# Optimization experiments

Measured on AMD Instinct MI355X. Metric: run time of the kernel, lower is better.

Reference implementation:

```python
import jax, jax.numpy as jnp
import numpy as np

N = 50000      # nodes per graph
E = 800000     # directed edges per graph
D_IN, C1, C2, C3, K = 96, 64, 32, 16, 16  # K = tensor_neurons (Linear(16,16) forces 16)


def setup_inputs() -> dict:
    key = jax.random.key(0)
    ks = jax.random.split(key, 18)
    def w(k, shape, scale=0.1):
        return (jax.random.normal(k, shape, jnp.float32) * scale)
    return {
        "features_1": jax.random.normal(ks[0], (N, D_IN), jnp.float32),
        "features_2": jax.random.normal(ks[1], (N, D_IN), jnp.float32),
        "edges_1": jax.random.randint(ks[2], (2, E), 0, N),
        "edges_2": jax.random.randint(ks[3], (2, E), 0, N),
        # GCN layer params (PyG GCNConv: X @ W then normalized aggregation, then + b)
        "W1": w(ks[4], (D_IN, C1)), "b1": jnp.zeros((C1,), jnp.float32),
        "W2": w(ks[5], (C1, C2)),  "b2": jnp.zeros((C2,), jnp.float32),
        "W3": w(ks[6], (C2, C3)),  "b3": jnp.zeros((C3,), jnp.float32),
        # Attention pooling weight matrix [C3, C3]
        "Wa": w(ks[7], (C3, C3)),
        # Tensor network: bilinear tensor [C3, C3, K], block [K, 2*C3], bias [K]
        "Wt": w(ks[8], (C3, C3, K)),
        "Wb": w(ks[9], (K, 2 * C3)),
        "bt": w(ks[10], (K,)),
        # fully_connected_first Linear(16,16) and scoring Linear(16,1)
        "Wfc": w(ks[11], (K, 16)), "bfc": jnp.zeros((16,), jnp.float32),
        "Wsc": w(ks[12], (16, 1)), "bsc": jnp.zeros((1,), jnp.float32),
    }


def gcn_conv(x, src, dst, W, b):
    # PyG GCNConv with self-loops: D^-1/2 (A+I) D^-1/2 (X W) + b
    h = x @ W                                   # [N, C]
    ones = jnp.ones(src.shape[0], h.dtype)
    deg = jax.ops.segment_sum(ones, dst, num_segments=N) + 1.0   # in-degree + self loop
    dinv = jax.lax.rsqrt(deg)                   # [N]
    coef = dinv[src] * dinv[dst]                # [E]
    agg = jax.ops.segment_sum(h[src] * coef[:, None], dst, num_segments=N)
    return agg + h * (dinv * dinv)[:, None] + b  # self-loop term has norm dinv_i^2


def encode(x, edges, W1, b1, W2, b2, W3, b3):
    src, dst = edges[0], edges[1]
    x = jax.nn.relu(gcn_conv(x, src, dst, W1, b1))  # dropout is a no-op in eval mode
    x = jax.nn.relu(gcn_conv(x, src, dst, W2, b2))
    return gcn_conv(x, src, dst, W3, b3)


def attention_pool(x, Wa):
    # SimGNN AttentionModule: c = tanh(mean(x Wa)); s = sigmoid(x c); rep = x^T s
    c = jnp.tanh(jnp.mean(x @ Wa, axis=0))      # [C3]
    s = jax.nn.sigmoid(x @ c)                   # [N]
    return x.T @ s                              # [C3]


def reference(features_1, features_2, edges_1, edges_2,
              W1, b1, W2, b2, W3, b3, Wa, Wt, Wb, bt, Wfc, bfc, Wsc, bsc):
    h1 = encode(features_1, edges_1, W1, b1, W2, b2, W3, b3)
    h2 = encode(features_2, edges_2, W1, b1, W2, b2, W3, b3)
    e1 = attention_pool(h1, Wa)                 # [C3]
    e2 = attention_pool(h2, Wa)                 # [C3]
    # Tensor network scoring
    bilinear = jnp.einsum('i,ijk,j->k', e1, Wt, e2)        # [K]
    block = Wb @ jnp.concatenate([e1, e2])                 # [K]
    scores = jax.nn.relu(bilinear + block + bt)            # [K]
    scores = jnp.tanh(scores @ Wfc + bfc)                  # [16]
    score = jax.nn.sigmoid(scores @ Wsc + bsc)             # [1]
    return score
```

## Files before the change

### kernel.cpp

```cpp
#include <hip/hip_runtime.h>
#include <hip/hip_bf16.h>

#define TPB 256
#define SH 6
#define BW 64

typedef unsigned short u16;
typedef __attribute__((ext_vector_type(8))) __bf16 bf16x8;
typedef __attribute__((ext_vector_type(4))) float f32x4;

__device__ __forceinline__ u16 f_to_bf(float f) {
    unsigned u = __float_as_uint(f);
    return (u16)((u + 0x7fff + ((u >> 16) & 1)) >> 16);
}
__device__ __forceinline__ float4 bf4_to_f4(ushort4 v) {
    float4 r;
    r.x = __uint_as_float((unsigned)v.x << 16);
    r.y = __uint_as_float((unsigned)v.y << 16);
    r.z = __uint_as_float((unsigned)v.z << 16);
    r.w = __uint_as_float((unsigned)v.w << 16);
    return r;
}
__device__ __forceinline__ void facc(float4& a, float4 v) {
    a.x += v.x; a.y += v.y; a.z += v.z; a.w += v.w;
}
__device__ __forceinline__ float4 shfl_xor4(float4 v, int mask, int width) {
    v.x = __shfl_xor(v.x, mask, width);
    v.y = __shfl_xor(v.y, mask, width);
    v.z = __shfl_xor(v.z, mask, width);
    v.w = __shfl_xor(v.w, mask, width);
    return v;
}

__device__ __forceinline__ bool swz_block(int nblk, int& g, int& bx) {
    int blk = blockIdx.x;
    int j = blk & 7;
    g = j >> 2;
    bx = (blk >> 3) * 4 + (j & 3);
    return bx < nblk;
}

template <int C>
__device__ __forceinline__ float4 gather_sum(const u16* __restrict__ HW,
                                             const int* __restrict__ col,
                                             int c0, int ps, int pe) {
    float4 a0 = make_float4(0.f, 0.f, 0.f, 0.f);
    float4 a1 = a0, a2 = a0, a3 = a0;
    int p = ps;
    for (; p + 8 <= pe; p += 8) {
        int j[8];
        ushort4 d[8];
#pragma unroll
        for (int k = 0; k < 8; k++) j[k] = col[p + k];
#pragma unroll
        for (int k = 0; k < 8; k++) d[k] = *(const ushort4*)&HW[(size_t)j[k] * C + c0];
        facc(a0, bf4_to_f4(d[0])); facc(a1, bf4_to_f4(d[1]));
        facc(a2, bf4_to_f4(d[2])); facc(a3, bf4_to_f4(d[3]));
        facc(a0, bf4_to_f4(d[4])); facc(a1, bf4_to_f4(d[5]));
        facc(a2, bf4_to_f4(d[6])); facc(a3, bf4_to_f4(d[7]));
    }
    if (p + 4 <= pe) {
        int j[4];
        ushort4 d[4];
#pragma unroll
        for (int k = 0; k < 4; k++) j[k] = col[p + k];
#pragma unroll
        for (int k = 0; k < 4; k++) d[k] = *(const ushort4*)&HW[(size_t)j[k] * C + c0];
        facc(a0, bf4_to_f4(d[0])); facc(a1, bf4_to_f4(d[1]));
        facc(a2, bf4_to_f4(d[2])); facc(a3, bf4_to_f4(d[3]));
        p += 4;
    }
    for (; p < pe; p++) {
        int j = col[p];
        facc(a0, bf4_to_f4(*(const ushort4*)&HW[(size_t)j * C + c0]));
    }
    facc(a0, a1); facc(a2, a3); facc(a0, a2);
    return a0;
}


__global__ void bucket_scatter_kernel(const int* __restrict__ e0, const int* __restrict__ e1,
                                      int E, int* __restrict__ bcur,
                                      int* __restrict__ ebuf0, int* __restrict__ ebuf1,
                                      int nbuk, int cap) {
    int g = blockIdx.y;
    const int* src = g ? e1 : e0;
    const int* dst = src + E;
    int* ebuf = g ? ebuf1 : ebuf0;
    int* bu = bcur + g * 1024;
    __shared__ int hist[1024];
    for (int t = threadIdx.x; t < 1024; t += TPB) hist[t] = 0;
    __syncthreads();
    int base = blockIdx.x * 4096;
    int pk[16], bk[16], rk[16];
#pragma unroll
    for (int k = 0; k < 16; k++) {
        int e = base + k * TPB + (int)threadIdx.x;
        bk[k] = -1;
        if (e < E) {
            int s = src[e], d = dst[e];
            int b = d >> SH;
            bk[k] = b;
            pk[k] = (s << SH) | (d & (BW - 1));
            rk[k] = atomicAdd(&hist[b], 1);
        }
    }
    __syncthreads();
    for (int t = threadIdx.x; t < nbuk; t += TPB) {
        int h = hist[t];
        hist[t] = h ? atomicAdd(&bu[t], h) : 0;
    }
    __syncthreads();
#pragma unroll
    for (int k = 0; k < 16; k++)
        if (bk[k] >= 0) {
            int pos = hist[bk[k]] + rk[k];
            if (pos < cap) ebuf[(size_t)bk[k] * cap + pos] = pk[k];
        }
}

__global__ void bucket_csr_kernel(const int* __restrict__ ebuf0, const int* __restrict__ ebuf1,
                                  const int* __restrict__ bcur, int n, int cap,
                                  int* __restrict__ soff0, int* __restrict__ soff1,
                                  int* __restrict__ eoff0, int* __restrict__ eoff1,
                                  float* __restrict__ dinv0, float* __restrict__ dinv1,
                                  int* __restrict__ col0, int* __restrict__ col1) {
    int g = blockIdx.y;
    int b = blockIdx.x;
    const int* ebuf = g ? ebuf1 : ebuf0;
    int* soff = g ? soff1 : soff0;
    int* eoff = g ? eoff1 : eoff0;
    float* dinv = g ? dinv1 : dinv0;
    int* col = g ? col1 : col0;
    __shared__ int h[BW], nb[BW], nrank[BW];
    int tid = threadIdx.x;
    if (tid < BW) h[tid] = 0;
    __syncthreads();
    int s = b * cap;
    int cnt = min(bcur[g * 1024 + b], cap);
    int e = s + cnt;
    for (int i = s + tid; i < e; i += TPB)
        atomicAdd(&h[ebuf[i] & (BW - 1)], 1);
    __syncthreads();
    if (tid < BW) {
        int v = h[tid];
        int x = v;
        for (int d = 1; d < BW; d <<= 1) {
            int u = __shfl_up(x, d, 64);
            if (tid >= d) x += u;
        }
        int base = s + x - v;
        nb[tid] = base;
        nrank[tid] = 0;
        int node = b * BW + tid;
        if (node < n) {
            soff[node] = base;
            eoff[node] = base + v;
            dinv[node] = rsqrtf((float)v + 1.0f);
        }
    }
    __syncthreads();
    for (int i = s + tid; i < e; i += TPB) {
        int p = ebuf[i];
        int lo = p & (BW - 1);
        int r = atomicAdd(&nrank[lo], 1);
        col[nb[lo] + r] = p >> SH;
    }
}


template <int CIN, int COUT>
__global__ void matmul_kernel(const float* __restrict__ X0, const float* __restrict__ X1,
                              const float* __restrict__ W,
                              const float* __restrict__ dinv0, const float* __restrict__ dinv1,
                              u16* __restrict__ Y0, u16* __restrict__ Y1, int n) {
    constexpr int CINP = CIN + 8;
    constexpr int NT = COUT / 16;
    constexpr int KT = CIN / 32;
    __shared__ u16 Xs[64 * CINP];
    __shared__ u16 Wt[COUT * CINP];

    int g = blockIdx.y;
    const float* X = g ? X1 : X0;
    const float* dinv = g ? dinv1 : dinv0;
    u16* Y = g ? Y1 : Y0;
    int nb0 = blockIdx.x * 64;

    for (int i = threadIdx.x; i < 64 * (CIN / 4); i += TPB) {
        int nn = i / (CIN / 4), kc = i % (CIN / 4);
        float4 v = make_float4(0.f, 0.f, 0.f, 0.f);
        if (nb0 + nn < n) v = *(const float4*)&X[(size_t)(nb0 + nn) * CIN + 4 * kc];
        ushort4 b;
        b.x = f_to_bf(v.x); b.y = f_to_bf(v.y); b.z = f_to_bf(v.z); b.w = f_to_bf(v.w);
        *(ushort4*)&Xs[nn * CINP + 4 * kc] = b;
    }
    for (int i = threadIdx.x; i < CIN * (COUT / 4); i += TPB) {
        int k = i / (COUT / 4), nc4 = i % (COUT / 4);
        float4 v = *(const float4*)&W[(size_t)k * COUT + 4 * nc4];
        Wt[(4 * nc4 + 0) * CINP + k] = f_to_bf(v.x);
        Wt[(4 * nc4 + 1) * CINP + k] = f_to_bf(v.y);
        Wt[(4 * nc4 + 2) * CINP + k] = f_to_bf(v.z);
        Wt[(4 * nc4 + 3) * CINP + k] = f_to_bf(v.w);
    }
    __syncthreads();

    int lane = threadIdx.x & 63;
    int w = threadIdx.x >> 6;
    int m = lane & 15;
    int quad = lane >> 4;

    f32x4 acc[NT];
#pragma unroll
    for (int t = 0; t < NT; t++) acc[t] = (f32x4){0.f, 0.f, 0.f, 0.f};
#pragma unroll
    for (int kt = 0; kt < KT; kt++) {
        int k0 = kt * 32 + quad * 8;
        bf16x8 a = *(const bf16x8*)&Xs[(w * 16 + m) * CINP + k0];
#pragma unroll
        for (int t = 0; t < NT; t++) {
            bf16x8 b = *(const bf16x8*)&Wt[(t * 16 + m) * CINP + k0];
            acc[t] = __builtin_amdgcn_mfma_f32_16x16x32_bf16(a, b, acc[t], 0, 0, 0);
        }
    }
#pragma unroll
    for (int r = 0; r < 4; r++) {
        int node = nb0 + w * 16 + quad * 4 + r;
        if (node < n) {
            float d = dinv[node];
#pragma unroll
            for (int t = 0; t < NT; t++)
                Y[(size_t)node * COUT + t * 16 + m] = f_to_bf(acc[t][r] * d);
        }
    }
}


template <int C, int SPLIT, int COUT2>
__global__ __launch_bounds__(TPB, 2)
void agg_mm_kernel(const u16* __restrict__ HW0, const u16* __restrict__ HW1,
                   const int* __restrict__ soff0, const int* __restrict__ soff1,
                   const int* __restrict__ eoff0, const int* __restrict__ eoff1,
                   const int* __restrict__ col0, const int* __restrict__ col1,
                   const float* __restrict__ dinv0, const float* __restrict__ dinv1,
                   const float* __restrict__ bias, const float* __restrict__ W2,
                   u16* __restrict__ Y0, u16* __restrict__ Y1, int n, int nblk) {
    constexpr int CH = C / 4;
    constexpr int TPN = CH * SPLIT;
    constexpr int CP = C + 8;
    constexpr int NT2 = COUT2 / 16;
    constexpr int KT2 = C / 32;
    __shared__ __align__(16) u16 HsB[16 * CP];
    __shared__ __align__(16) u16 WtB[COUT2 * CP];

    int g, bx;
    if (!swz_block(nblk, g, bx)) return;
    const u16* HW = g ? HW1 : HW0;
    const int* soff = g ? soff1 : soff0;
    const int* eoff = g ? eoff1 : eoff0;
    const int* col = g ? col1 : col0;
    const float* dinv = g ? dinv1 : dinv0;
    u16* Y = g ? Y1 : Y0;

    for (int idx = threadIdx.x; idx < C * COUT2; idx += TPB) {
        int k = idx / COUT2, nc = idx % COUT2;
        WtB[nc * CP + k] = f_to_bf(W2[idx]);
    }

    int tid = bx * TPB + (int)threadIdx.x;
    int node = tid / TPN;
    int nl = threadIdx.x / TPN;
    int part = threadIdx.x % TPN;
    int sp = part / CH;
    int c0 = (part % CH) * 4;
    float4 o = make_float4(0.f, 0.f, 0.f, 0.f);
    if (node < n) {
        int s = soff[node], e = eoff[node];
        int len = e - s;
        int chunk = (len + SPLIT - 1) / SPLIT;
        int ps = s + sp * chunk;
        int pe = min(ps + chunk, e);
        float4 r = gather_sum<C>(HW, col, c0, ps, pe);
#pragma unroll
        for (int m = CH; m < TPN; m <<= 1) facc(r, shfl_xor4(r, m, TPN));
        if (sp == 0) {
            float di = dinv[node];
            float4 self = bf4_to_f4(*(const ushort4*)&HW[(size_t)node * C + c0]);
            float4 b4 = *(const float4*)&bias[c0];
            o.x = fmaxf(di * (r.x + self.x) + b4.x, 0.f);
            o.y = fmaxf(di * (r.y + self.y) + b4.y, 0.f);
            o.z = fmaxf(di * (r.z + self.z) + b4.z, 0.f);
            o.w = fmaxf(di * (r.w + self.w) + b4.w, 0.f);
        }
    }
    if (sp == 0) {
        ushort4 hb;
        hb.x = f_to_bf(o.x); hb.y = f_to_bf(o.y); hb.z = f_to_bf(o.z); hb.w = f_to_bf(o.w);
        *(ushort4*)&HsB[nl * CP + c0] = hb;
    }
    __syncthreads();

    int lane = threadIdx.x & 63;
    int w = threadIdx.x >> 6;
    if (w < NT2) {
        int m = lane & 15;
        int quad = lane >> 4;
        f32x4 acc = (f32x4){0.f, 0.f, 0.f, 0.f};
#pragma unroll
        for (int kt = 0; kt < KT2; kt++) {
            int k0 = kt * 32 + quad * 8;
            bf16x8 a = *(const bf16x8*)&HsB[m * CP + k0];
            bf16x8 b = *(const bf16x8*)&WtB[(w * 16 + m) * CP + k0];
            acc = __builtin_amdgcn_mfma_f32_16x16x32_bf16(a, b, acc, 0, 0, 0);
        }
        int base16 = bx * 16;
#pragma unroll
        for (int r = 0; r < 4; r++) {
            int onode = base16 + quad * 4 + r;
            if (onode < n)
                Y[(size_t)onode * COUT2 + w * 16 + m] = f_to_bf(acc[r] * dinv[onode]);
        }
    }
}

__global__ __launch_bounds__(TPB, 2)
void agg16_kernel(const u16* __restrict__ HW0, const u16* __restrict__ HW1,
                  const int* __restrict__ soff0, const int* __restrict__ soff1,
                  const int* __restrict__ eoff0, const int* __restrict__ eoff1,
                  const int* __restrict__ col0, const int* __restrict__ col1,
                  const float* __restrict__ dinv0, const float* __restrict__ dinv1,
                  const float* __restrict__ bias,
                  float* __restrict__ out0, float* __restrict__ out1,
                  float* __restrict__ pcol, int n, int nblk) {
    int g, bx;
    if (!swz_block(nblk, g, bx)) return;
    const u16* HW = g ? HW1 : HW0;
    const int* soff = g ? soff1 : soff0;
    const int* eoff = g ? eoff1 : eoff0;
    const int* col = g ? col1 : col0;
    const float* dinv = g ? dinv1 : dinv0;
    float* outp = g ? out1 : out0;
    int tid = bx * TPB + (int)threadIdx.x;
    int node = tid / 16;
    int part = tid % 16;
    int sp = part / 4;
    int c0 = (part % 4) * 4;
    float4 o = make_float4(0.f, 0.f, 0.f, 0.f);
    if (node < n) {
        int s = soff[node], e = eoff[node];
        int len = e - s;
        int chunk = (len + 3) / 4;
        int ps = s + sp * chunk;
        int pe = min(ps + chunk, e);
        float4 r = gather_sum<16>(HW, col, c0, ps, pe);
        facc(r, shfl_xor4(r, 4, 16));
        facc(r, shfl_xor4(r, 8, 16));
        if (sp == 0) {
            float di = dinv[node];
            float4 self = bf4_to_f4(*(const ushort4*)&HW[(size_t)node * 16 + c0]);
            float4 b4 = *(const float4*)&bias[c0];
            o.x = di * (r.x + self.x) + b4.x;
            o.y = di * (r.y + self.y) + b4.y;
            o.z = di * (r.z + self.z) + b4.z;
            o.w = di * (r.w + self.w) + b4.w;
            *(float4*)&outp[(size_t)node * 16 + c0] = o;
        }
    }
    __shared__ float4 sd[TPB];
    sd[threadIdx.x] = (node < n && sp == 0) ? o : make_float4(0.f, 0.f, 0.f, 0.f);
    __syncthreads();
    if (threadIdx.x < 64) {
        float4 a = sd[threadIdx.x];
        facc(a, sd[threadIdx.x + 64]);
        facc(a, sd[threadIdx.x + 128]);
        facc(a, sd[threadIdx.x + 192]);
        sd[threadIdx.x] = a;
    }
    __syncthreads();
    if (threadIdx.x < 16) {
        float4 a = sd[threadIdx.x];
        facc(a, sd[threadIdx.x + 16]);
        facc(a, sd[threadIdx.x + 32]);
        facc(a, sd[threadIdx.x + 48]);
        sd[threadIdx.x] = a;
    }
    __syncthreads();
    if (threadIdx.x < 4)
        *(float4*)&pcol[((size_t)g * nblk + bx) * 16 + threadIdx.x * 4] = sd[threadIdx.x];
}


__global__ void cvec_kernel(const float* __restrict__ pcol, int nb16, float n_inv,
                            const float* __restrict__ Wa, float* __restrict__ cvec) {
    int g = blockIdx.x;
    const float4* p4 = (const float4*)(pcol + (size_t)g * nb16 * 16);
    __shared__ float4 sd[TPB];
    __shared__ float cs[16];
    int c4 = threadIdx.x & 3;
    int row = threadIdx.x >> 2;
    float4 acc = make_float4(0.f, 0.f, 0.f, 0.f);
    for (int r = row; r < nb16; r += 64) facc(acc, p4[(size_t)r * 4 + c4]);
    sd[threadIdx.x] = acc;
    __syncthreads();
    if (threadIdx.x < 64) {
        float4 a = sd[threadIdx.x];
        facc(a, sd[threadIdx.x + 64]);
        facc(a, sd[threadIdx.x + 128]);
        facc(a, sd[threadIdx.x + 192]);
        sd[threadIdx.x] = a;
    }
    __syncthreads();
    if (threadIdx.x < 16) {
        float4 a = sd[threadIdx.x];
        facc(a, sd[threadIdx.x + 16]);
        facc(a, sd[threadIdx.x + 32]);
        facc(a, sd[threadIdx.x + 48]);
        sd[threadIdx.x] = a;
    }
    __syncthreads();
    if (threadIdx.x < 4) {
        float4 a = sd[threadIdx.x];
        facc(a, sd[threadIdx.x + 4]);
        facc(a, sd[threadIdx.x + 8]);
        facc(a, sd[threadIdx.x + 12]);
        cs[threadIdx.x * 4 + 0] = a.x * n_inv;
        cs[threadIdx.x * 4 + 1] = a.y * n_inv;
        cs[threadIdx.x * 4 + 2] = a.z * n_inv;
        cs[threadIdx.x * 4 + 3] = a.w * n_inv;
    }
    __syncthreads();
    if (threadIdx.x < 16) {
        float acc2 = 0.f;
#pragma unroll
        for (int i = 0; i < 16; i++) acc2 += cs[i] * Wa[i * 16 + threadIdx.x];
        cvec[g * 16 + threadIdx.x] = tanhf(acc2);
    }
}


__global__ void pool_kernel(const float* __restrict__ H0, const float* __restrict__ H1, int n,
                            const float* __restrict__ cvec, float* __restrict__ ppool) {
    int g = blockIdx.y;
    const float* H = g ? H1 : H0;
    int c = threadIdx.x & 15;
    float cv = cvec[g * 16 + c];
    int w = (blockIdx.x * blockDim.x + threadIdx.x) / 16;
    int stride = (gridDim.x * blockDim.x) / 16;
    float acc = 0.f;
    for (int node = w; node < n; node += stride) {
        float x = H[(size_t)node * 16 + c];
        float p = x * cv;
        p += __shfl_xor(p, 1, 16);
        p += __shfl_xor(p, 2, 16);
        p += __shfl_xor(p, 4, 16);
        p += __shfl_xor(p, 8, 16);
        float s = 1.f / (1.f + __expf(-p));
        acc += s * x;
    }
    __shared__ float sdata[TPB];
    sdata[threadIdx.x] = acc;
    __syncthreads();
    if (threadIdx.x < 16) {
        float s = 0.f;
        for (int t = threadIdx.x; t < TPB; t += 16) s += sdata[t];
        ppool[((size_t)g * gridDim.x + blockIdx.x) * 16 + threadIdx.x] = s;
    }
}


__global__ void final_kernel(const float* __restrict__ ppool, int nbp,
                             const float* __restrict__ Wt, const float* __restrict__ Wb,
                             const float* __restrict__ bt, const float* __restrict__ Wfc,
                             const float* __restrict__ bfc, const float* __restrict__ Wsc,
                             const float* __restrict__ bsc, float* __restrict__ out) {
    __shared__ float4 sd4[TPB];
    __shared__ float rep[32], part[TPB], scores[16], tvec[16];
    int t = threadIdx.x;
    {
        const float4* p4 = (const float4*)ppool;
        int g = t >> 7;
        int r0 = (t >> 2) & 31;
        int c4 = t & 3;
        float4 acc = make_float4(0.f, 0.f, 0.f, 0.f);
        for (int r = r0; r < nbp; r += 32)
            facc(acc, p4[((size_t)g * nbp + r) * 4 + c4]);
        sd4[t] = acc;
        __syncthreads();
        for (int st = 16; st >= 1; st >>= 1) {
            if (r0 < st) facc(sd4[t], sd4[t + st * 4]);
            __syncthreads();
        }
        if (r0 == 0) {
            float4 a = sd4[t];
            rep[g * 16 + c4 * 4 + 0] = a.x;
            rep[g * 16 + c4 * 4 + 1] = a.y;
            rep[g * 16 + c4 * 4 + 2] = a.z;
            rep[g * 16 + c4 * 4 + 3] = a.w;
        }
        __syncthreads();
    }
    {
        int p = t >> 4, tt = t & 15;
        float b = 0.f;
#pragma unroll
        for (int q = 0; q < 16; q++)
            b += rep[q] * Wt[(q * 16 + p) * 16 + tt];
        part[t] = b * rep[16 + p];
    }
    __syncthreads();
    if (t < 16) {
        float bil = 0.f;
#pragma unroll
        for (int p = 0; p < 16; p++) bil += part[p * 16 + t];
        float blk = 0.f;
#pragma unroll
        for (int m = 0; m < 16; m++)
            blk += Wb[t * 32 + m] * rep[m] + Wb[t * 32 + 16 + m] * rep[16 + m];
        scores[t] = fmaxf(bil + blk + bt[t], 0.f);
    }
    __syncthreads();
    if (t < 16) {
        float acc = bfc[t];
#pragma unroll
        for (int k = 0; k < 16; k++) acc += scores[k] * Wfc[k * 16 + t];
        tvec[t] = tanhf(acc);
    }
    __syncthreads();
    if (t == 0) {
        float acc = bsc[0];
#pragma unroll
        for (int j = 0; j < 16; j++) acc += tvec[j] * Wsc[j];
        out[0] = 1.f / (1.f + __expf(-acc));
    }
}


extern "C" void kernel_launch(void* const* d_in, const int* in_sizes, int n_in,
                              void* d_out, int out_size, void* d_ws, size_t ws_size,
                              hipStream_t stream) {
    const float* X1 = (const float*)d_in[0];
    const float* X2 = (const float*)d_in[1];
    const int* edges1 = (const int*)d_in[2];
    const int* edges2 = (const int*)d_in[3];
    const float* W1 = (const float*)d_in[4];
    const float* b1 = (const float*)d_in[5];
    const float* W2 = (const float*)d_in[6];
    const float* b2 = (const float*)d_in[7];
    const float* W3 = (const float*)d_in[8];
    const float* b3 = (const float*)d_in[9];
    const float* Wa = (const float*)d_in[10];
    const float* Wt = (const float*)d_in[11];
    const float* Wb = (const float*)d_in[12];
    const float* bt = (const float*)d_in[13];
    const float* Wfc = (const float*)d_in[14];
    const float* bfc = (const float*)d_in[15];
    const float* Wsc = (const float*)d_in[16];
    const float* bsc = (const float*)d_in[17];
    float* out = (float*)d_out;

    const int N = in_sizes[0] / 96;
    const int E = in_sizes[2] / 2;
    const int NBUK = (N + BW - 1) / BW;
    int cap = ((2 * (E / NBUK)) + 255) & ~255;
    if (cap < 256) cap = 256;

    char* ws = (char*)d_ws;
    size_t o = 0;
    auto alloc = [&](size_t bytes) {
        void* p = ws + o;
        o += (bytes + 255) & ~(size_t)255;
        return p;
    };
    int* bcur = (int*)alloc((size_t)2 * 1024 * 4);
    int* soff0 = (int*)alloc((size_t)N * 4);
    int* soff1 = (int*)alloc((size_t)N * 4);
    int* eoff0 = (int*)alloc((size_t)N * 4);
    int* eoff1 = (int*)alloc((size_t)N * 4);
    int* col0 = (int*)alloc((size_t)NBUK * cap * 4);
    int* col1 = (int*)alloc((size_t)NBUK * cap * 4);
    int* ebuf0 = (int*)alloc((size_t)NBUK * cap * 4);
    int* ebuf1 = (int*)alloc((size_t)NBUK * cap * 4);
    float* dinv0 = (float*)alloc((size_t)N * 4);
    float* dinv1 = (float*)alloc((size_t)N * 4);
    u16* hwbA0 = (u16*)alloc((size_t)N * 64 * 2);
    u16* hwbA1 = (u16*)alloc((size_t)N * 64 * 2);
    u16* hwbB0 = (u16*)alloc((size_t)N * 32 * 2);
    u16* hwbB1 = (u16*)alloc((size_t)N * 32 * 2);
    u16* hwbC0 = (u16*)alloc((size_t)N * 16 * 2);
    u16* hwbC1 = (u16*)alloc((size_t)N * 16 * 2);
    float* H30 = (float*)alloc((size_t)N * 16 * 4);
    float* H31 = (float*)alloc((size_t)N * 16 * 4);

    const int gB2 = (E + 4095) / 4096;
    const int g16 = ((size_t)N * 16 + TPB - 1) / TPB;
    const int gSwz = 8 * ((g16 + 3) / 4);
    const int gMM = (N + 63) / 64;
    const int gPool = 256;

    float* pcol = (float*)alloc((size_t)2 * g16 * 16 * 4);
    float* cvecArr = (float*)alloc(32 * 4);
    float* ppool = (float*)alloc((size_t)2 * gPool * 16 * 4);

    hipMemsetAsync(bcur, 0, (size_t)2 * 1024 * 4, stream);

    bucket_scatter_kernel<<<dim3(gB2, 2), TPB, 0, stream>>>(edges1, edges2, E, bcur,
                                                            ebuf0, ebuf1, NBUK, cap);
    bucket_csr_kernel<<<dim3(NBUK, 2), TPB, 0, stream>>>(ebuf0, ebuf1, bcur, N, cap,
                                                         soff0, soff1, eoff0, eoff1,
                                                         dinv0, dinv1, col0, col1);

    matmul_kernel<96, 64><<<dim3(gMM, 2), TPB, 0, stream>>>(X1, X2, W1, dinv0, dinv1, hwbA0, hwbA1, N);
    agg_mm_kernel<64, 1, 32><<<gSwz, TPB, 0, stream>>>(
        hwbA0, hwbA1, soff0, soff1, eoff0, eoff1, col0, col1, dinv0, dinv1, b1, W2,
        hwbB0, hwbB1, N, g16);
    agg_mm_kernel<32, 2, 16><<<gSwz, TPB, 0, stream>>>(
        hwbB0, hwbB1, soff0, soff1, eoff0, eoff1, col0, col1, dinv0, dinv1, b2, W3,
        hwbC0, hwbC1, N, g16);
    agg16_kernel<<<gSwz, TPB, 0, stream>>>(
        hwbC0, hwbC1, soff0, soff1, eoff0, eoff1, col0, col1, dinv0, dinv1, b3,
        H30, H31, pcol, N, g16);

    cvec_kernel<<<2, TPB, 0, stream>>>(pcol, g16, 1.0f / (float)N, Wa, cvecArr);
    pool_kernel<<<dim3(gPool, 2), TPB, 0, stream>>>(H30, H31, N, cvecArr, ppool);
    final_kernel<<<1, 256, 0, stream>>>(ppool, gPool, Wt, Wb, bt, Wfc, bfc, Wsc, bsc, out);
}
```

Baseline: 261.0 us.

## Split layer-1 aggregation into channel planes and unfuse the W2 matmul

The first matmul now writes its 64-channel output as two 32-channel planes. A new aggregation kernel gathers each plane separately, mapped to XCD groups, so every gathered row is 64 bytes and fits better in per-XCD caches. The layer-1 output (bias plus ReLU) is stored as bf16 to a new buffer, and a separate bf16-input matmul kernel applies W2, replacing the fused agg_mm step. This adds an extra kernel launch and a round trip of a 64-channel intermediate through memory, in exchange for better gather locality.

```diff
diff --git a/kernel.cpp b/kernel.cpp
--- a/kernel.cpp
+++ b/kernel.cpp
@@ -169,7 +169,7 @@
 }
 
 
-template <int CIN, int COUT>
+template <int CIN, int COUT, bool PLANES>
 __global__ void matmul_kernel(const float* __restrict__ X0, const float* __restrict__ X1,
                               const float* __restrict__ W,
                               const float* __restrict__ dinv0, const float* __restrict__ dinv1,
@@ -228,9 +228,131 @@
         if (node < n) {
             float d = dinv[node];
 #pragma unroll
+            for (int t = 0; t < NT; t++) {
+                if constexpr (PLANES) {
+                    size_t idx = (size_t)(t >> 1) * ((size_t)n * (COUT / 2)) +
+                                 (size_t)node * (COUT / 2) + (t & 1) * 16 + m;
+                    Y[idx] = f_to_bf(acc[t][r] * d);
+                } else {
+                    Y[(size_t)node * COUT + t * 16 + m] = f_to_bf(acc[t][r] * d);
+                }
+            }
+        }
+    }
+}
+
+
+template <int CIN, int COUT>
+__global__ void matmul_bf_kernel(const u16* __restrict__ X0, const u16* __restrict__ X1,
+                                 const float* __restrict__ W,
+                                 const float* __restrict__ dinv0, const float* __restrict__ dinv1,
+                                 u16* __restrict__ Y0, u16* __restrict__ Y1, int n) {
+    constexpr int CINP = CIN + 8;
+    constexpr int NT = COUT / 16;
+    constexpr int KT = CIN / 32;
+    __shared__ u16 Xs[64 * CINP];
+    __shared__ u16 Wt[COUT * CINP];
+
+    int g = blockIdx.y;
+    const u16* X = g ? X1 : X0;
+    const float* dinv = g ? dinv1 : dinv0;
+    u16* Y = g ? Y1 : Y0;
+    int nb0 = blockIdx.x * 64;
+
+    for (int i = threadIdx.x; i < 64 * (CIN / 8); i += TPB) {
+        int nn = i / (CIN / 8), kc = i % (CIN / 8);
+        ulonglong2 v = {0ull, 0ull};
+        if (nb0 + nn < n) v = *(const ulonglong2*)&X[(size_t)(nb0 + nn) * CIN + 8 * kc];
+        *(ulonglong2*)&Xs[nn * CINP + 8 * kc] = v;
+    }
+    for (int i = threadIdx.x; i < CIN * (COUT / 4); i += TPB) {
+        int k = i / (COUT / 4), nc4 = i % (COUT / 4);
+        float4 v = *(const float4*)&W[(size_t)k * COUT + 4 * nc4];
+        Wt[(4 * nc4 + 0) * CINP + k] = f_to_bf(v.x);
+        Wt[(4 * nc4 + 1) * CINP + k] = f_to_bf(v.y);
+        Wt[(4 * nc4 + 2) * CINP + k] = f_to_bf(v.z);
+        Wt[(4 * nc4 + 3) * CINP + k] = f_to_bf(v.w);
+    }
+    __syncthreads();
+
+    int lane = threadIdx.x & 63;
+    int w = threadIdx.x >> 6;
+    int m = lane & 15;
+    int quad = lane >> 4;
+
+    f32x4 acc[NT];
+#pragma unroll
+    for (int t = 0; t < NT; t++) acc[t] = (f32x4){0.f, 0.f, 0.f, 0.f};
+#pragma unroll
+    for (int kt = 0; kt < KT; kt++) {
+        int k0 = kt * 32 + quad * 8;
+        bf16x8 a = *(const bf16x8*)&Xs[(w * 16 + m) * CINP + k0];
+#pragma unroll
+        for (int t = 0; t < NT; t++) {
+            bf16x8 b = *(const bf16x8*)&Wt[(t * 16 + m) * CINP + k0];
+            acc[t] = __builtin_amdgcn_mfma_f32_16x16x32_bf16(a, b, acc[t], 0, 0, 0);
+        }
+    }
+#pragma unroll
+    for (int r = 0; r < 4; r++) {
+        int node = nb0 + w * 16 + quad * 4 + r;
+        if (node < n) {
+            float d = dinv[node];
+#pragma unroll
             for (int t = 0; t < NT; t++)
                 Y[(size_t)node * COUT + t * 16 + m] = f_to_bf(acc[t][r] * d);
         }
+    }
+}
+
+
+__global__ __launch_bounds__(TPB, 2)
+void agg_split_kernel(const u16* __restrict__ P0, const u16* __restrict__ P1,
+                      const int* __restrict__ soff0, const int* __restrict__ soff1,
+                      const int* __restrict__ eoff0, const int* __restrict__ eoff1,
+                      const int* __restrict__ col0, const int* __restrict__ col1,
+                      const float* __restrict__ dinv0, const float* __restrict__ dinv1,
+                      const float* __restrict__ bias,
+                      u16* __restrict__ H0, u16* __restrict__ H1, int n, int nblk) {
+    int blk = blockIdx.x;
+    int xcd = blk & 7;
+    int g = xcd >> 2;
+    int ch = (xcd >> 1) & 1;
+    int bx = (blk >> 3) * 2 + (xcd & 1);
+    if (bx >= nblk) return;
+    const u16* P = (g ? P1 : P0) + (size_t)ch * n * 32;
+    const int* soff = g ? soff1 : soff0;
+    const int* eoff = g ? eoff1 : eoff0;
+    const int* col = g ? col1 : col0;
+    const float* dinv = g ? dinv1 : dinv0;
+    u16* H = g ? H1 : H0;
+
+    int nl = threadIdx.x >> 4;
+    int part = threadIdx.x & 15;
+    int sp = part >> 3;
+    int c0 = (part & 7) * 4;
+    int node = bx * 16 + nl;
+    if (node >= n) return;
+
+    int s = soff[node], e = eoff[node];
+    int len = e - s;
+    int chunk = (len + 1) >> 1;
+    int ps = s + sp * chunk;
+    int pe = min(ps + chunk, e);
+    float4 r = gather_sum<32>(P, col, c0, ps, pe);
+    facc(r, shfl_xor4(r, 8, 16));
+    if (sp == 0) {
+        float di = dinv[node];
+        float4 self = bf4_to_f4(*(const ushort4*)&P[(size_t)node * 32 + c0]);
+        float4 b4 = *(const float4*)&bias[ch * 32 + c0];
+        float4 o;
+        o.x = fmaxf(di * (r.x + self.x) + b4.x, 0.f);
+        o.y = fmaxf(di * (r.y + self.y) + b4.y, 0.f);
+        o.z = fmaxf(di * (r.z + self.z) + b4.z, 0.f);
+        o.w = fmaxf(di * (r.w + self.w) + b4.w, 0.f);
+        ushort4 hb;
+        hb.x = f_to_bf(o.x); hb.y = f_to_bf(o.y); hb.z = f_to_bf(o.z); hb.w = f_to_bf(o.w);
+        *(ushort4*)&H[(size_t)node * 64 + ch * 32 + c0] = hb;
     }
 }
 
@@ -583,6 +705,8 @@
     float* dinv1 = (float*)alloc((size_t)N * 4);
     u16* hwbA0 = (u16*)alloc((size_t)N * 64 * 2);
     u16* hwbA1 = (u16*)alloc((size_t)N * 64 * 2);
+    u16* hwbH0 = (u16*)alloc((size_t)N * 64 * 2);
+    u16* hwbH1 = (u16*)alloc((size_t)N * 64 * 2);
     u16* hwbB0 = (u16*)alloc((size_t)N * 32 * 2);
     u16* hwbB1 = (u16*)alloc((size_t)N * 32 * 2);
     u16* hwbC0 = (u16*)alloc((size_t)N * 16 * 2);
@@ -593,6 +717,7 @@
     const int gB2 = (E + 4095) / 4096;
     const int g16 = ((size_t)N * 16 + TPB - 1) / TPB;
     const int gSwz = 8 * ((g16 + 3) / 4);
+    const int gSplit = 8 * ((g16 + 1) / 2);
     const int gMM = (N + 63) / 64;
     const int gPool = 256;
 
@@ -608,10 +733,13 @@
                                                          soff0, soff1, eoff0, eoff1,
                                                          dinv0, dinv1, col0, col1);
 
-    matmul_kernel<96, 64><<<dim3(gMM, 2), TPB, 0, stream>>>(X1, X2, W1, dinv0, dinv1, hwbA0, hwbA1, N);
-    agg_mm_kernel<64, 1, 32><<<gSwz, TPB, 0, stream>>>(
-        hwbA0, hwbA1, soff0, soff1, eoff0, eoff1, col0, col1, dinv0, dinv1, b1, W2,
-        hwbB0, hwbB1, N, g16);
+    matmul_kernel<96, 64, true><<<dim3(gMM, 2), TPB, 0, stream>>>(
+        X1, X2, W1, dinv0, dinv1, hwbA0, hwbA1, N);
+    agg_split_kernel<<<gSplit, TPB, 0, stream>>>(
+        hwbA0, hwbA1, soff0, soff1, eoff0, eoff1, col0, col1, dinv0, dinv1, b1,
+        hwbH0, hwbH1, N, g16);
+    matmul_bf_kernel<64, 32><<<dim3(gMM, 2), TPB, 0, stream>>>(
+        hwbH0, hwbH1, W2, dinv0, dinv1, hwbB0, hwbB1, N);
     agg_mm_kernel<32, 2, 16><<<gSwz, TPB, 0, stream>>>(
         hwbB0, hwbB1, soff0, soff1, eoff0, eoff1, col0, col1, dinv0, dinv1, b2, W3,
         hwbC0, hwbC1, N, g16);
```

Result: slower. 271.9 us (+4.2%).

## Widen gather loads to 16-byte bf16x8 with edge-parity split; store layer-3 output as bf16

Applied to the files above, without the earlier changes.

The neighbor gather in the aggregation kernels now reads 8 bf16 values per thread as one uint4 load instead of 4 via ushort4. Each node's 16 threads are remapped into channel chunks times an even/odd edge split plus the SPLIT partitions, and partial sums are combined with shuffle reductions over 8 floats. The final GCN layer output is also stored as bf16 rather than fp32, which halves the traffic for the pool kernel. The costs are more shuffle reductions, more registers per thread, and lower precision in the pooled features.

```diff
diff --git a/kernel.cpp b/kernel.cpp
--- a/kernel.cpp
+++ b/kernel.cpp
@@ -13,23 +13,8 @@
     unsigned u = __float_as_uint(f);
     return (u16)((u + 0x7fff + ((u >> 16) & 1)) >> 16);
 }
-__device__ __forceinline__ float4 bf4_to_f4(ushort4 v) {
-    float4 r;
-    r.x = __uint_as_float((unsigned)v.x << 16);
-    r.y = __uint_as_float((unsigned)v.y << 16);
-    r.z = __uint_as_float((unsigned)v.z << 16);
-    r.w = __uint_as_float((unsigned)v.w << 16);
-    return r;
-}
 __device__ __forceinline__ void facc(float4& a, float4 v) {
     a.x += v.x; a.y += v.y; a.z += v.z; a.w += v.w;
-}
-__device__ __forceinline__ float4 shfl_xor4(float4 v, int mask, int width) {
-    v.x = __shfl_xor(v.x, mask, width);
-    v.y = __shfl_xor(v.y, mask, width);
-    v.z = __shfl_xor(v.z, mask, width);
-    v.w = __shfl_xor(v.w, mask, width);
-    return v;
 }
 
 __device__ __forceinline__ bool swz_block(int nblk, int& g, int& bx) {
@@ -40,42 +25,46 @@
     return bx < nblk;
 }
 
+__device__ __forceinline__ void acc8_add(float* __restrict__ a, uint4 d) {
+    a[0] += __uint_as_float(d.x << 16);
+    a[1] += __uint_as_float(d.x & 0xffff0000u);
+    a[2] += __uint_as_float(d.y << 16);
+    a[3] += __uint_as_float(d.y & 0xffff0000u);
+    a[4] += __uint_as_float(d.z << 16);
+    a[5] += __uint_as_float(d.z & 0xffff0000u);
+    a[6] += __uint_as_float(d.w << 16);
+    a[7] += __uint_as_float(d.w & 0xffff0000u);
+}
+
 template <int C>
-__device__ __forceinline__ float4 gather_sum(const u16* __restrict__ HW,
+__device__ __forceinline__ void gather_sum16(const u16* __restrict__ HW,
                                              const int* __restrict__ col,
-                                             int c0, int ps, int pe) {
-    float4 a0 = make_float4(0.f, 0.f, 0.f, 0.f);
-    float4 a1 = a0, a2 = a0, a3 = a0;
+                                             int e, int c8, int ps, int pe,
+                                             float* __restrict__ acc) {
     int p = ps;
     for (; p + 8 <= pe; p += 8) {
-        int j[8];
-        ushort4 d[8];
-#pragma unroll
-        for (int k = 0; k < 8; k++) j[k] = col[p + k];
-#pragma unroll
-        for (int k = 0; k < 8; k++) d[k] = *(const ushort4*)&HW[(size_t)j[k] * C + c0];
-        facc(a0, bf4_to_f4(d[0])); facc(a1, bf4_to_f4(d[1]));
-        facc(a2, bf4_to_f4(d[2])); facc(a3, bf4_to_f4(d[3]));
-        facc(a0, bf4_to_f4(d[4])); facc(a1, bf4_to_f4(d[5]));
-        facc(a2, bf4_to_f4(d[6])); facc(a3, bf4_to_f4(d[7]));
-    }
-    if (p + 4 <= pe) {
         int j[4];
-        ushort4 d[4];
-#pragma unroll
-        for (int k = 0; k < 4; k++) j[k] = col[p + k];
-#pragma unroll
-        for (int k = 0; k < 4; k++) d[k] = *(const ushort4*)&HW[(size_t)j[k] * C + c0];
-        facc(a0, bf4_to_f4(d[0])); facc(a1, bf4_to_f4(d[1]));
-        facc(a2, bf4_to_f4(d[2])); facc(a3, bf4_to_f4(d[3]));
-        p += 4;
-    }
-    for (; p < pe; p++) {
+        uint4 d[4];
+#pragma unroll
+        for (int r = 0; r < 4; r++) j[r] = col[p + 2 * r + e];
+#pragma unroll
+        for (int r = 0; r < 4; r++) d[r] = *(const uint4*)&HW[(size_t)j[r] * C + c8 * 8];
+#pragma unroll
+        for (int r = 0; r < 4; r++) acc8_add(acc, d[r]);
+    }
+    for (; p + 2 <= pe; p += 2) {
+        int j = col[p + e];
+        acc8_add(acc, *(const uint4*)&HW[(size_t)j * C + c8 * 8]);
+    }
+    if (p < pe && e == 0) {
         int j = col[p];
-        facc(a0, bf4_to_f4(*(const ushort4*)&HW[(size_t)j * C + c0]));
-    }
-    facc(a0, a1); facc(a2, a3); facc(a0, a2);
-    return a0;
+        acc8_add(acc, *(const uint4*)&HW[(size_t)j * C + c8 * 8]);
+    }
+}
+
+__device__ __forceinline__ void red8(float* __restrict__ a, int mask, int width) {
+#pragma unroll
+    for (int i = 0; i < 8; i++) a[i] += __shfl_xor(a[i], mask, width);
 }
 
 
@@ -244,8 +233,9 @@
                    const float* __restrict__ dinv0, const float* __restrict__ dinv1,
                    const float* __restrict__ bias, const float* __restrict__ W2,
                    u16* __restrict__ Y0, u16* __restrict__ Y1, int n, int nblk) {
-    constexpr int CH = C / 4;
-    constexpr int TPN = CH * SPLIT;
+    constexpr int CHUNKS = C / 8;
+    constexpr int GRP = 2 * CHUNKS;
+    constexpr int TPN = GRP * SPLIT;
     constexpr int CP = C + 8;
     constexpr int NT2 = COUT2 / 16;
     constexpr int KT2 = C / 32;
@@ -266,36 +256,53 @@
         WtB[nc * CP + k] = f_to_bf(W2[idx]);
     }
 
-    int tid = bx * TPB + (int)threadIdx.x;
-    int node = tid / TPN;
-    int nl = threadIdx.x / TPN;
-    int part = threadIdx.x % TPN;
-    int sp = part / CH;
-    int c0 = (part % CH) * 4;
-    float4 o = make_float4(0.f, 0.f, 0.f, 0.f);
+    int nl = threadIdx.x >> 4;
+    int part = threadIdx.x & 15;
+    int sp = part / GRP;
+    int gl = part % GRP;
+    int e = gl / CHUNKS;
+    int c8 = gl % CHUNKS;
+    int node = bx * 16 + nl;
+
+    float acc[8];
+#pragma unroll
+    for (int i = 0; i < 8; i++) acc[i] = 0.f;
+    float o8[8];
+#pragma unroll
+    for (int i = 0; i < 8; i++) o8[i] = 0.f;
+
     if (node < n) {
-        int s = soff[node], e = eoff[node];
-        int len = e - s;
+        int s = soff[node], en = eoff[node];
+        int len = en - s;
         int chunk = (len + SPLIT - 1) / SPLIT;
         int ps = s + sp * chunk;
-        int pe = min(ps + chunk, e);
-        float4 r = gather_sum<C>(HW, col, c0, ps, pe);
-#pragma unroll
-        for (int m = CH; m < TPN; m <<= 1) facc(r, shfl_xor4(r, m, TPN));
-        if (sp == 0) {
+        int pe = min(ps + chunk, en);
+        gather_sum16<C>(HW, col, e, c8, ps, pe, acc);
+        red8(acc, CHUNKS, TPN);
+#pragma unroll
+        for (int m = GRP; m < TPN; m <<= 1) red8(acc, m, TPN);
+        if (part < CHUNKS) {
             float di = dinv[node];
-            float4 self = bf4_to_f4(*(const ushort4*)&HW[(size_t)node * C + c0]);
-            float4 b4 = *(const float4*)&bias[c0];
-            o.x = fmaxf(di * (r.x + self.x) + b4.x, 0.f);
-            o.y = fmaxf(di * (r.y + self.y) + b4.y, 0.f);
-            o.z = fmaxf(di * (r.z + self.z) + b4.z, 0.f);
-            o.w = fmaxf(di * (r.w + self.w) + b4.w, 0.f);
-        }
-    }
-    if (sp == 0) {
-        ushort4 hb;
-        hb.x = f_to_bf(o.x); hb.y = f_to_bf(o.y); hb.z = f_to_bf(o.z); hb.w = f_to_bf(o.w);
-        *(ushort4*)&HsB[nl * CP + c0] = hb;
+            uint4 sv = *(const uint4*)&HW[(size_t)node * C + part * 8];
+            float4 b0 = *(const float4*)&bias[part * 8];
+            float4 b1 = *(const float4*)&bias[part * 8 + 4];
+            o8[0] = fmaxf(di * (acc[0] + __uint_as_float(sv.x << 16)) + b0.x, 0.f);
+            o8[1] = fmaxf(di * (acc[1] + __uint_as_float(sv.x & 0xffff0000u)) + b0.y, 0.f);
+            o8[2] = fmaxf(di * (acc[2] + __uint_as_float(sv.y << 16)) + b0.z, 0.f);
+            o8[3] = fmaxf(di * (acc[3] + __uint_as_float(sv.y & 0xffff0000u)) + b0.w, 0.f);
+            o8[4] = fmaxf(di * (acc[4] + __uint_as_float(sv.z << 16)) + b1.x, 0.f);
+            o8[5] = fmaxf(di * (acc[5] + __uint_as_float(sv.z & 0xffff0000u)) + b1.y, 0.f);
+            o8[6] = fmaxf(di * (acc[6] + __uint_as_float(sv.w << 16)) + b1.z, 0.f);
+            o8[7] = fmaxf(di * (acc[7] + __uint_as_float(sv.w & 0xffff0000u)) + b1.w, 0.f);
+        }
+    }
+    if (part < CHUNKS) {
+        uint4 hv;
+        hv.x = (unsigned)f_to_bf(o8[0]) | ((unsigned)f_to_bf(o8[1]) << 16);
+        hv.y = (unsigned)f_to_bf(o8[2]) | ((unsigned)f_to_bf(o8[3]) << 16);
+        hv.z = (unsigned)f_to_bf(o8[4]) | ((unsigned)f_to_bf(o8[5]) << 16);
+        hv.w = (unsigned)f_to_bf(o8[6]) | ((unsigned)f_to_bf(o8[7]) << 16);
+        *(uint4*)&HsB[nl * CP + part * 8] = hv;
     }
     __syncthreads();
 
@@ -304,20 +311,20 @@
     if (w < NT2) {
         int m = lane & 15;
         int quad = lane >> 4;
-        f32x4 acc = (f32x4){0.f, 0.f, 0.f, 0.f};
+        f32x4 ac = (f32x4){0.f, 0.f, 0.f, 0.f};
 #pragma unroll
         for (int kt = 0; kt < KT2; kt++) {
             int k0 = kt * 32 + quad * 8;
             bf16x8 a = *(const bf16x8*)&HsB[m * CP + k0];
             bf16x8 b = *(const bf16x8*)&WtB[(w * 16 + m) * CP + k0];
-            acc = __builtin_amdgcn_mfma_f32_16x16x32_bf16(a, b, acc, 0, 0, 0);
+            ac = __builtin_amdgcn_mfma_f32_16x16x32_bf16(a, b, ac, 0, 0, 0);
         }
         int base16 = bx * 16;
 #pragma unroll
         for (int r = 0; r < 4; r++) {
             int onode = base16 + quad * 4 + r;
             if (onode < n)
-                Y[(size_t)onode * COUT2 + w * 16 + m] = f_to_bf(acc[r] * dinv[onode]);
+                Y[(size_t)onode * COUT2 + w * 16 + m] = f_to_bf(ac[r] * dinv[onode]);
         }
     }
 }
@@ -329,7 +336,7 @@
                   const int* __restrict__ col0, const int* __restrict__ col1,
                   const float* __restrict__ dinv0, const float* __restrict__ dinv1,
                   const float* __restrict__ bias,
-                  float* __restrict__ out0, float* __restrict__ out1,
+                  u16* __restrict__ out0, u16* __restrict__ out1,
                   float* __restrict__ pcol, int n, int nblk) {
     int g, bx;
     if (!swz_block(nblk, g, bx)) return;
@@ -338,54 +345,82 @@
     const int* eoff = g ? eoff1 : eoff0;
     const int* col = g ? col1 : col0;
     const float* dinv = g ? dinv1 : dinv0;
-    float* outp = g ? out1 : out0;
-    int tid = bx * TPB + (int)threadIdx.x;
-    int node = tid / 16;
-    int part = tid % 16;
-    int sp = part / 4;
-    int c0 = (part % 4) * 4;
-    float4 o = make_float4(0.f, 0.f, 0.f, 0.f);
+    u16* outp = g ? out1 : out0;
+
+    int nl = threadIdx.x >> 4;
+    int part = threadIdx.x & 15;
+    int sp = part >> 2;
+    int gl = part & 3;
+    int e = gl >> 1;
+    int c8 = gl & 1;
+    int node = bx * 16 + nl;
+
+    float acc[8];
+#pragma unroll
+    for (int i = 0; i < 8; i++) acc[i] = 0.f;
+    float o8[8];
+#pragma unroll
+    for (int i = 0; i < 8; i++) o8[i] = 0.f;
+
     if (node < n) {
-        int s = soff[node], e = eoff[node];
-        int len = e - s;
-        int chunk = (len + 3) / 4;
+        int s = soff[node], en = eoff[node];
+        int len = en - s;
+        int chunk = (len + 3) >> 2;
         int ps = s + sp * chunk;
-        int pe = min(ps + chunk, e);
-        float4 r = gather_sum<16>(HW, col, c0, ps, pe);
-        facc(r, shfl_xor4(r, 4, 16));
-        facc(r, shfl_xor4(r, 8, 16));
-        if (sp == 0) {
+        int pe = min(ps + chunk, en);
+        gather_sum16<16>(HW, col, e, c8, ps, pe, acc);
+        red8(acc, 2, 16);
+        red8(acc, 4, 16);
+        red8(acc, 8, 16);
+        if (part < 2) {
             float di = dinv[node];
-            float4 self = bf4_to_f4(*(const ushort4*)&HW[(size_t)node * 16 + c0]);
-            float4 b4 = *(const float4*)&bias[c0];
-            o.x = di * (r.x + self.x) + b4.x;
-            o.y = di * (r.y + self.y) + b4.y;
-            o.z = di * (r.z + self.z) + b4.z;
-            o.w = di * (r.w + self.w) + b4.w;
-            *(float4*)&outp[(size_t)node * 16 + c0] = o;
-        }
-    }
-    __shared__ float4 sd[TPB];
-    sd[threadIdx.x] = (node < n && sp == 0) ? o : make_float4(0.f, 0.f, 0.f, 0.f);
+            uint4 sv = *(const uint4*)&HW[(size_t)node * 16 + part * 8];
+            float4 b0 = *(const float4*)&bias[part * 8];
+            float4 b1 = *(const float4*)&bias[part * 8 + 4];
+            o8[0] = di * (acc[0] + __uint_as_float(sv.x << 16)) + b0.x;
+            o8[1] = di * (acc[1] + __uint_as_float(sv.x & 0xffff0000u)) + b0.y;
+            o8[2] = di * (acc[2] + __uint_as_float(sv.y << 16)) + b0.z;
+            o8[3] = di * (acc[3] + __uint_as_float(sv.y & 0xffff0000u)) + b0.w;
+            o8[4] = di * (acc[4] + __uint_as_float(sv.z << 16)) + b1.x;
+            o8[5] = di * (acc[5] + __uint_as_float(sv.z & 0xffff0000u)) + b1.y;
+            o8[6] = di * (acc[6] + __uint_as_float(sv.w << 16)) + b1.z;
+            o8[7] = di * (acc[7] + __uint_as_float(sv.w & 0xffff0000u)) + b1.w;
+            uint4 hv;
+            hv.x = (unsigned)f_to_bf(o8[0]) | ((unsigned)f_to_bf(o8[1]) << 16);
+            hv.y = (unsigned)f_to_bf(o8[2]) | ((unsigned)f_to_bf(o8[3]) << 16);
+            hv.z = (unsigned)f_to_bf(o8[4]) | ((unsigned)f_to_bf(o8[5]) << 16);
+            hv.w = (unsigned)f_to_bf(o8[6]) | ((unsigned)f_to_bf(o8[7]) << 16);
+            *(uint4*)&outp[(size_t)node * 16 + part * 8] = hv;
+        }
+    }
+    __shared__ float4 sa[TPB], sb[TPB];
+    bool hold = (node < n) && (part < 2);
+    sa[threadIdx.x] = hold ? make_float4(o8[0], o8[1], o8[2], o8[3])
+                           : make_float4(0.f, 0.f, 0.f, 0.f);
+    sb[threadIdx.x] = hold ? make_float4(o8[4], o8[5], o8[6], o8[7])
+                           : make_float4(0.f, 0.f, 0.f, 0.f);
     __syncthreads();
     if (threadIdx.x < 64) {
-        float4 a = sd[threadIdx.x];
-        facc(a, sd[threadIdx.x + 64]);
-        facc(a, sd[threadIdx.x + 128]);
-        facc(a, sd[threadIdx.x + 192]);
-        sd[threadIdx.x] = a;
+        float4 a = sa[threadIdx.x], b = sb[threadIdx.x];
+        facc(a, sa[threadIdx.x + 64]);  facc(b, sb[threadIdx.x + 64]);
+        facc(a, sa[threadIdx.x + 128]); facc(b, sb[threadIdx.x + 128]);
+        facc(a, sa[threadIdx.x + 192]); facc(b, sb[threadIdx.x + 192]);
+        sa[threadIdx.x] = a; sb[threadIdx.x] = b;
     }
     __syncthreads();
     if (threadIdx.x < 16) {
-        float4 a = sd[threadIdx.x];
-        facc(a, sd[threadIdx.x + 16]);
-        facc(a, sd[threadIdx.x + 32]);
-        facc(a, sd[threadIdx.x + 48]);
-        sd[threadIdx.x] = a;
-    }
-    __syncthreads();
-    if (threadIdx.x < 4)
-        *(float4*)&pcol[((size_t)g * nblk + bx) * 16 + threadIdx.x * 4] = sd[threadIdx.x];
+        float4 a = sa[threadIdx.x], b = sb[threadIdx.x];
+        facc(a, sa[threadIdx.x + 16]); facc(b, sb[threadIdx.x + 16]);
+        facc(a, sa[threadIdx.x + 32]); facc(b, sb[threadIdx.x + 32]);
+        facc(a, sa[threadIdx.x + 48]); facc(b, sb[threadIdx.x + 48]);
+        sa[threadIdx.x] = a; sb[threadIdx.x] = b;
+    }
+    __syncthreads();
+    if (threadIdx.x < 2) {
+        float* dst = &pcol[((size_t)g * nblk + bx) * 16 + threadIdx.x * 8];
+        *(float4*)&dst[0] = sa[threadIdx.x];
+        *(float4*)&dst[4] = sb[threadIdx.x];
+    }
 }
 
 
@@ -437,17 +472,17 @@
 }
 
 
-__global__ void pool_kernel(const float* __restrict__ H0, const float* __restrict__ H1, int n,
+__global__ void pool_kernel(const u16* __restrict__ H0, const u16* __restrict__ H1, int n,
                             const float* __restrict__ cvec, float* __restrict__ ppool) {
     int g = blockIdx.y;
-    const float* H = g ? H1 : H0;
+    const u16* H = g ? H1 : H0;
     int c = threadIdx.x & 15;
     float cv = cvec[g * 16 + c];
     int w = (blockIdx.x * blockDim.x + threadIdx.x) / 16;
     int stride = (gridDim.x * blockDim.x) / 16;
     float acc = 0.f;
     for (int node = w; node < n; node += stride) {
-        float x = H[(size_t)node * 16 + c];
+        float x = __uint_as_float((unsigned)H[(size_t)node * 16 + c] << 16);
         float p = x * cv;
         p += __shfl_xor(p, 1, 16);
         p += __shfl_xor(p, 2, 16);
@@ -587,8 +622,8 @@
     u16* hwbB1 = (u16*)alloc((size_t)N * 32 * 2);
     u16* hwbC0 = (u16*)alloc((size_t)N * 16 * 2);
     u16* hwbC1 = (u16*)alloc((size_t)N * 16 * 2);
-    float* H30 = (float*)alloc((size_t)N * 16 * 4);
-    float* H31 = (float*)alloc((size_t)N * 16 * 4);
+    u16* H30 = (u16*)alloc((size_t)N * 16 * 2);
+    u16* H31 = (u16*)alloc((size_t)N * 16 * 2);
 
     const int gB2 = (E + 4095) / 4096;
     const int g16 = ((size_t)N * 16 + TPB - 1) / TPB;
@@ -608,7 +643,8 @@
                                                          soff0, soff1, eoff0, eoff1,
                                                          dinv0, dinv1, col0, col1);
 
-    matmul_kernel<96, 64><<<dim3(gMM, 2), TPB, 0, stream>>>(X1, X2, W1, dinv0, dinv1, hwbA0, hwbA1, N);
+    matmul_kernel<96, 64><<<dim3(gMM, 2), TPB, 0, stream>>>(X1, X2, W1, dinv0, dinv1,
+                                                            hwbA0, hwbA1, N);
     agg_mm_kernel<64, 1, 32><<<gSwz, TPB, 0, stream>>>(
         hwbA0, hwbA1, soff0, soff1, eoff0, eoff1, col0, col1, dinv0, dinv1, b1, W2,
         hwbB0, hwbB1, N, g16);
```

Measured after the change: 256.7 us. Within noise of the previous version (-1.7%).
